# Optimization experiments

Hardware: AMD Instinct MI355X
Metric: run time of the kernel (lower is better)

## Reference

```python
import jax, jax.numpy as jnp
import numpy as np

D_MODEL = 1024
N_HEADS = 16
HEAD_DIM = D_MODEL // N_HEADS
Q_PROJ = D_MODEL // 2
KV_PROJ = D_MODEL
INIT_SCALE = 0.02
EPS = 1e-5


def _ln(x, g, b):
    mu = jnp.mean(x, axis=-1, keepdims=True)
    var = jnp.mean(jnp.square(x - mu), axis=-1, keepdims=True)
    return (x - mu) * jax.lax.rsqrt(var + EPS) * g + b


def setup_inputs() -> dict:
    key = jax.random.key(0)
    ks = jax.random.split(key, 8)
    B, S = 2, 2048
    x = jax.random.normal(ks[0], (B, S, D_MODEL), dtype=jnp.float32)
    W_dq = INIT_SCALE * jax.random.normal(ks[1], (D_MODEL, Q_PROJ), dtype=jnp.float32)
    W_uq = INIT_SCALE * jax.random.normal(ks[2], (Q_PROJ, D_MODEL), dtype=jnp.float32)
    W_dkv = INIT_SCALE * jax.random.normal(ks[3], (D_MODEL, KV_PROJ), dtype=jnp.float32)
    W_ukv = INIT_SCALE * jax.random.normal(ks[4], (KV_PROJ, 2 * D_MODEL), dtype=jnp.float32)
    wo = INIT_SCALE * jax.random.normal(ks[5], (D_MODEL, D_MODEL), dtype=jnp.float32)
    return {
        "x": x,
        "W_dq": W_dq, "W_uq": W_uq,
        "q_ln_g": jnp.ones((Q_PROJ,), jnp.float32), "q_ln_b": jnp.zeros((Q_PROJ,), jnp.float32),
        "W_dkv": W_dkv, "W_ukv": W_ukv,
        "kv_ln_g": jnp.ones((KV_PROJ,), jnp.float32), "kv_ln_b": jnp.zeros((KV_PROJ,), jnp.float32),
        "preq_g": jnp.ones((D_MODEL,), jnp.float32), "preq_b": jnp.zeros((D_MODEL,), jnp.float32),
        "prekv_g": jnp.ones((D_MODEL,), jnp.float32), "prekv_b": jnp.zeros((D_MODEL,), jnp.float32),
        "wo": wo,
    }


def reference(x, W_dq, W_uq, q_ln_g, q_ln_b, W_dkv, W_ukv, kv_ln_g, kv_ln_b,
              preq_g, preq_b, prekv_g, prekv_b, wo):
    B, S, D = x.shape
    H, dh = N_HEADS, HEAD_DIM
    # Q path: pre-norm -> low-rank down -> LN -> up
    x_q = _ln(x, preq_g, preq_b)
    cq = _ln(x_q @ W_dq, q_ln_g, q_ln_b)            # [B,S,D/2]
    Q = (cq @ W_uq).reshape(B, S, H, dh)             # [B,S,H,dh]
    Q = Q / jnp.sqrt(jnp.asarray(dh, x.dtype))
    # KV path: pre-norm -> compress -> LN -> up, split into K,V
    x_kv = _ln(x, prekv_g, prekv_b)
    ckv = _ln(x_kv @ W_dkv, kv_ln_g, kv_ln_b)        # [B,S,D]
    KV = ckv @ W_ukv                                 # [B,S,2D]
    K, V = jnp.split(KV, 2, axis=-1)
    K = K.reshape(B, S, H, dh)
    V = V.reshape(B, S, H, dh)
    # causal attention (scores materialized as in original)
    scores = jnp.einsum('bqhd,bkhd->bhqk', Q, K)     # [B,H,S,S]
    causal = jnp.tril(jnp.ones((S, S), dtype=bool))  # True where allowed
    scores = jnp.where(causal[None, None], scores, jnp.asarray(-jnp.inf, scores.dtype))
    attn = jax.nn.softmax(scores, axis=-1)
    out = jnp.einsum('bhqk,bkhd->bqhd', attn, V).reshape(B, S, D)
    return out @ wo.T
```

## Files before the change

kernel.cpp:

```cpp
#include <hip/hip_runtime.h>
#include <hip/hip_bf16.h>

#define SEQ   2048
#define BATCH 2
#define NROWS 4096
#define DM    1024
#define NHEAD 16
#define DH    64
#define QP    512
#define KVP   1024
#define CH    8

typedef unsigned short us;
typedef ushort4 us4;
using bf16x8 = __attribute__((ext_vector_type(8))) __bf16;
using f32x4  = __attribute__((ext_vector_type(4))) float;

__device__ __forceinline__ us f2bf(float f) {
  union { __hip_bfloat16 h; us u; } cv;
  cv.h = __float2bfloat16(f);
  return cv.u;
}
__device__ __forceinline__ float bf2f(us u) {
  union { unsigned int u32; float f; } cv;
  cv.u32 = ((unsigned int)u) << 16;
  return cv.f;
}
__device__ __forceinline__ float loadp(const void* p, long i, int isbf) {
  return isbf ? bf2f(((const us*)p)[i]) : ((const float*)p)[i];
}
__device__ __forceinline__ void async16(const void* g, void* l) {
  __builtin_amdgcn_global_load_lds((__attribute__((address_space(1))) void*)g,
                                   (__attribute__((address_space(3))) void*)l,
                                   16, 0, 0);
}

__global__ void detect_dtype(const us* __restrict__ xu, int* __restrict__ flag,
                             float4* __restrict__ zsmall, int nz4) {
  __shared__ int red[256];
  const int tid = threadIdx.x;
  const float4 z = {0.f, 0.f, 0.f, 0.f};
  for (int i = tid; i < nz4; i += 256) zsmall[i] = z;
  int cnt = 0;
  for (int i = tid; i < 4096; i += 256) {
    const int e = (xu[i] >> 7) & 0xff;
    if (e == 0 || (e >= 100 && e <= 134)) cnt++;
  }
  red[tid] = cnt;
  __syncthreads();
  for (int s = 128; s; s >>= 1) {
    if (tid < s) red[tid] += red[tid + s];
    __syncthreads();
  }
  if (tid == 0) *flag = (red[0] >= 3900) ? 1 : 0;
}

struct TD { const void* in; us* out; int R, C, nt, trans;
            const void* g; const void* b; float* u; float* c; };

__global__ __launch_bounds__(256) void stage0(
    TD t0, TD t1, TD t2, TD t3, TD t4,
    float4* __restrict__ zp, int n4,
    const void* __restrict__ xin,
    const void* __restrict__ g1, const void* __restrict__ b1,
    const void* __restrict__ g2, const void* __restrict__ b2,
    us* __restrict__ out1, us* __restrict__ out2,
    const int* __restrict__ flag)
{
  __shared__ us tile[32][33];
  __shared__ float red[8];
  __shared__ float musd[2];
  const int tid = threadIdx.x;
  const int isbf = *flag;
  int lin = blockIdx.x;

  if (lin < 5120) {
    TD t = t0;
    if (lin >= t.nt) { lin -= t.nt; t = t1;
      if (lin >= t.nt) { lin -= t.nt; t = t2;
        if (lin >= t.nt) { lin -= t.nt; t = t3;
          if (lin >= t.nt) { lin -= t.nt; t = t4; } } } }
    const int ntx = t.C >> 5;
    const int by = lin / ntx, bx = lin - by * ntx;
    const int tx = tid & 31, ty = tid >> 5;
    const long r0 = (long)by * 32, c0 = (long)bx * 32;
    if (t.trans) {
#pragma unroll
      for (int i = 0; i < 32; i += 8)
        tile[ty + i][tx] = isbf ? ((const us*)t.in)[(r0 + ty + i) * t.C + c0 + tx]
                                : f2bf(((const float*)t.in)[(r0 + ty + i) * t.C + c0 + tx]);
      __syncthreads();
      if (t.g) {
        const float gw = loadp(t.g, r0 + tx, isbf);
#pragma unroll
        for (int i = 0; i < 32; i += 8)
          t.out[(c0 + ty + i) * t.R + r0 + tx] = f2bf(bf2f(tile[tx][ty + i]) * gw);
        if (ty == 0) {
          float up = 0.f, cp = 0.f;
          for (int r = 0; r < 32; r++) {
            const float w = bf2f(tile[r][tx]);
            up += loadp(t.g, r0 + r, isbf) * w;
            cp += loadp(t.b, r0 + r, isbf) * w;
          }
          atomicAdd(&t.u[c0 + tx], up);
          atomicAdd(&t.c[c0 + tx], cp);
        }
      } else {
#pragma unroll
        for (int i = 0; i < 32; i += 8)
          t.out[(c0 + ty + i) * t.R + r0 + tx] = tile[tx][ty + i];
      }
    } else {
#pragma unroll
      for (int i = 0; i < 32; i += 8)
        t.out[(r0 + ty + i) * t.C + c0 + tx] =
            isbf ? ((const us*)t.in)[(r0 + ty + i) * t.C + c0 + tx]
                 : f2bf(((const float*)t.in)[(r0 + ty + i) * t.C + c0 + tx]);
    }
    return;
  }
  if (lin < 6144) {
    const float4 z = {0.f, 0.f, 0.f, 0.f};
    for (int i = (lin - 5120) * 256 + tid; i < n4; i += 1024 * 256) zp[i] = z;
    return;
  }
  const long row = lin - 6144;
  float v[4];
  float s = 0.f, s2 = 0.f;
#pragma unroll
  for (int i = 0; i < 4; i++) {
    const long c = tid + i * 256;
    const float t = loadp(xin, row * 1024 + c, isbf);
    v[i] = t; s += t; s2 += t * t;
  }
#pragma unroll
  for (int off = 32; off > 0; off >>= 1) {
    s  += __shfl_down(s,  off);
    s2 += __shfl_down(s2, off);
  }
  const int wave = tid >> 6, lane = tid & 63;
  if (lane == 0) { red[wave] = s; red[4 + wave] = s2; }
  __syncthreads();
  if (tid == 0) {
    const float ts = red[0] + red[1] + red[2] + red[3];
    const float t2 = red[4] + red[5] + red[6] + red[7];
    const float mu = ts * (1.f / 1024.f);
    const float var = t2 * (1.f / 1024.f) - mu * mu;
    musd[0] = mu; musd[1] = rsqrtf(var + 1e-5f);
  }
  __syncthreads();
  const float mu = musd[0], rs = musd[1];
#pragma unroll
  for (int i = 0; i < 4; i++) {
    const long c = tid + i * 256;
    const float nrm = (v[i] - mu) * rs;
    out1[row * 1024 + c] = f2bf(nrm * loadp(g1, c, isbf) + loadp(b1, c, isbf));
    out2[row * 1024 + c] = f2bf(nrm * loadp(g2, c, isbf) + loadp(b2, c, isbf));
  }
}

struct GD { const us* A; const us* Bt; void* C; int N, K, nxs; float scale; int omode;
            float* S1; float* S2; const float* u; const float* cv; us* C2; };

__global__ __launch_bounds__(256) void gemm_mt(GD g0, GD g1, int nb0,
                                               const int* __restrict__ flag) {
  __shared__ us As[2][128 * 32];
  __shared__ us Bs[2][128 * 32];
  GD g;
  int lin = blockIdx.x;
  if (lin < nb0) g = g0; else { g = g1; lin -= nb0; }
  const int by = lin >> g.nxs;
  const int bx = lin - (by << g.nxs);
  const int N = g.N, K = g.K;

  const int tid  = threadIdx.x;
  const int lane = tid & 63;
  const int wave = tid >> 6;
  const int n16  = lane & 15;
  const int quad = lane >> 4;
  const long m0 = (long)by * 128;
  const long n0 = (long)bx * 128;
  const int wm = (wave >> 1) * 64;
  const int wn = (wave & 1) * 64;

  const f32x4 zero = {0.f, 0.f, 0.f, 0.f};
  f32x4 acc[4][4];
#pragma unroll
  for (int i = 0; i < 4; i++)
#pragma unroll
    for (int j = 0; j < 4; j++) acc[i][j] = zero;

  const int srow = tid >> 2;
  const int scol = (tid & 3) * 8;
  const us* Ag0 = g.A  + (m0 + srow) * K + scol;
  const us* Ag1 = g.A  + (m0 + 64 + srow) * K + scol;
  const us* Bg0 = g.Bt + (n0 + srow) * K + scol;
  const us* Bg1 = g.Bt + (n0 + 64 + srow) * K + scol;
  const int lds_off = srow * 32 + scol;

  for (int k0 = 0; k0 < K; k0 += 64) {
#pragma unroll
    for (int s = 0; s < 2; s++) {
      const int ks = k0 + s * 32;
      async16(Ag0 + ks, As[s] + lds_off);
      async16(Ag1 + ks, As[s] + 2048 + lds_off);
      async16(Bg0 + ks, Bs[s] + lds_off);
      async16(Bg1 + ks, Bs[s] + 2048 + lds_off);
    }
    __syncthreads();
#pragma unroll
    for (int s = 0; s < 2; s++) {
      bf16x8 af[4], bfv[4];
#pragma unroll
      for (int i = 0; i < 4; i++)
        af[i] = *(const bf16x8*)(As[s] + (wm + i * 16 + n16) * 32 + quad * 8);
#pragma unroll
      for (int j = 0; j < 4; j++)
        bfv[j] = *(const bf16x8*)(Bs[s] + (wn + j * 16 + n16) * 32 + quad * 8);
#pragma unroll
      for (int i = 0; i < 4; i++)
#pragma unroll
        for (int j = 0; j < 4; j++)
          acc[i][j] = __builtin_amdgcn_mfma_f32_16x16x32_bf16(af[i], bfv[j], acc[i][j], 0, 0, 0);
    }
    __syncthreads();
  }

  const int om = g.omode;
  us* Cb = (us*)g.C;

  if (om == 4) {
    float s1a[4][4], s2a[4][4];
#pragma unroll
    for (int i = 0; i < 4; i++)
#pragma unroll
      for (int r = 0; r < 4; r++) { s1a[i][r] = 0.f; s2a[i][r] = 0.f; }
#pragma unroll
    for (int i = 0; i < 4; i++) {
      const long row = m0 + wm + i * 16 + quad * 4;
#pragma unroll
      for (int j = 0; j < 4; j++) {
        const long col = n0 + wn + j * 16 + n16;
#pragma unroll
        for (int r = 0; r < 4; r++) {
          const float v = acc[i][j][r] * g.scale;
          Cb[(row + r) * N + col] = f2bf(v);
          s1a[i][r] += v;
          s2a[i][r] += v * v;
        }
      }
    }
#pragma unroll
    for (int i = 0; i < 4; i++)
#pragma unroll
      for (int r = 0; r < 4; r++) {
        float a = s1a[i][r], b = s2a[i][r];
#pragma unroll
        for (int off = 1; off < 16; off <<= 1) {
          a += __shfl_xor(a, off);
          b += __shfl_xor(b, off);
        }
        if (n16 == 0) {
          const long row = m0 + wm + i * 16 + quad * 4 + r;
          atomicAdd(&g.S1[row], a);
          atomicAdd(&g.S2[row], b);
        }
      }
    return;
  }

  if (om == 5 || om == 6) {
    const float invK = 1.f / (float)K;
    float rsr[4][4], mur[4][4];
#pragma unroll
    for (int i = 0; i < 4; i++) {
      const long row = m0 + wm + i * 16 + quad * 4;
#pragma unroll
      for (int r = 0; r < 4; r++) {
        const float s1 = g.S1[row + r];
        const float s2 = g.S2[row + r];
        const float mu = s1 * invK;
        const float var = s2 * invK - mu * mu;
        const float rs = rsqrtf(var + 1e-5f);
        rsr[i][r] = rs;
        mur[i][r] = mu * rs;
      }
    }
    const bool vhalf = (om == 6) && (n0 >= 1024);
#pragma unroll
    for (int i = 0; i < 4; i++) {
      const long rowb = m0 + wm + i * 16 + quad * 4;
#pragma unroll
      for (int j = 0; j < 4; j++) {
        const long col = n0 + wn + j * 16 + n16;
        const float uu = g.u[col];
        const float cc = g.cv[col];
        if (!vhalf) {
          const int nst = (om == 6) ? 1024 : N;
#pragma unroll
          for (int r = 0; r < 4; r++) {
            const float v = g.scale * (rsr[i][r] * acc[i][j][r] - mur[i][r] * uu + cc);
            Cb[(rowb + r) * nst + col] = f2bf(v);
          }
        } else {
          const int bbq = (int)(rowb >> 11);
          const int key = (int)(rowb & 2047);
          const int dimg = (int)col - 1024;
          us4 pk;
          pk.x = f2bf(g.scale * (rsr[i][0] * acc[i][j][0] - mur[i][0] * uu + cc));
          pk.y = f2bf(g.scale * (rsr[i][1] * acc[i][j][1] - mur[i][1] * uu + cc));
          pk.z = f2bf(g.scale * (rsr[i][2] * acc[i][j][2] - mur[i][2] * uu + cc));
          pk.w = f2bf(g.scale * (rsr[i][3] * acc[i][j][3] - mur[i][3] * uu + cc));
          *(us4*)(g.C2 + ((long)(bbq * 1024 + dimg)) * 2048 + key) = pk;
        }
      }
    }
    return;
  }

  const bool obf = (om == 1) || (om == 2 && *flag != 0);
  float* Cf = (float*)g.C;
#pragma unroll
  for (int i = 0; i < 4; i++) {
    const long row = m0 + wm + i * 16 + quad * 4;
#pragma unroll
    for (int j = 0; j < 4; j++) {
      const long col = n0 + wn + j * 16 + n16;
#pragma unroll
      for (int r = 0; r < 4; r++) {
        const float v = acc[i][j][r] * g.scale;
        if (obf) Cb[(row + r) * N + col] = f2bf(v);
        else     Cf[(row + r) * N + col] = v;
      }
    }
  }
}

__global__ __launch_bounds__(256) void flash_attn(
    const us* __restrict__ Kbuf, const us* __restrict__ VT,
    const us* __restrict__ Q,
    float* __restrict__ Oacc, float* __restrict__ Lacc)
{
  __shared__ us Ks[64 * 72];
  __shared__ us Vt[64 * 72];
  __shared__ us Ps[4][32 * 72];

  int lin = blockIdx.x;
  int qt = 15, nc = 0;
  for (; qt >= 0; --qt) { nc = ((2 * qt + 1) >> 3) + 1; if (lin < nc) break; lin -= nc; }
  const int kt0 = lin * CH;
  const int kt1 = min(kt0 + CH, 2 * qt + 2);

  const int h   = blockIdx.y;
  const int bb  = blockIdx.z;
  const int tid = threadIdx.x;
  const int lane = tid & 63;
  const int wave = tid >> 6;
  const int n16 = lane & 15;
  const int quad = lane >> 4;
  const int qbase = qt * 128;
  const long rowQ0 = (long)bb * SEQ;

  bf16x8 aq[2][2];
#pragma unroll
  for (int rg = 0; rg < 2; rg++) {
    const long gq = (rowQ0 + qbase + wave * 32 + rg * 16 + n16) * DM + h * DH;
    aq[rg][0] = *(const bf16x8*)(Q + gq + quad * 8);
    aq[rg][1] = *(const bf16x8*)(Q + gq + 32 + quad * 8);
  }

  const f32x4 zero = {0.f, 0.f, 0.f, 0.f};
  f32x4 oacc[2][4];
#pragma unroll
  for (int rg = 0; rg < 2; rg++)
#pragma unroll
    for (int d = 0; d < 4; d++) oacc[rg][d] = zero;
  float rsum[2] = {0.f, 0.f};

  const int kk_key = tid >> 3;
  const int kk_d8  = (tid & 7) * 8;
  const int vd  = tid & 63;
  const int vkb = (tid >> 6) * 8;

  const us* kgb = Kbuf + (rowQ0 + kk_key) * 1024 + h * DH + kk_d8;
  const us* vtb = VT + ((long)bb * 1024 + h * DH + vd) * 2048;

  uint4 kpre0, kpre1, vpre0, vpre1;
  auto loadKV = [&](int kt) {
    const us* kg = kgb + (long)kt * (64 * 1024);
    kpre0 = *(const uint4*)kg;
    kpre1 = *(const uint4*)(kg + 32 * 1024);
    const us* vg = vtb + kt * 64 + vkb;
    vpre0 = *(const uint4*)vg;
    vpre1 = *(const uint4*)(vg + 32);
  };
  loadKV(kt0);

  us* Pw = Ps[wave];
  const int qw = qbase + wave * 32;

  for (int kt = kt0; kt < kt1; kt++) {
    const int kb = kt * 64;
    __syncthreads();
    *(uint4*)(Ks + kk_key * 72 + kk_d8)        = kpre0;
    *(uint4*)(Ks + (kk_key + 32) * 72 + kk_d8) = kpre1;
    *(uint4*)(Vt + vd * 72 + vkb)              = vpre0;
    *(uint4*)(Vt + vd * 72 + vkb + 32)         = vpre1;
    __syncthreads();
    if (kt + 1 < kt1) loadKV(kt + 1);

    if (kb > qw + 31) continue;

    f32x4 sv[2][4];
#pragma unroll
    for (int j = 0; j < 4; j++) {
      const bf16x8 ak0 = *(const bf16x8*)(Ks + (j * 16 + n16) * 72 + quad * 8);
      const bf16x8 ak1 = *(const bf16x8*)(Ks + (j * 16 + n16) * 72 + 32 + quad * 8);
#pragma unroll
      for (int rg = 0; rg < 2; rg++) {
        f32x4 s = zero;
        s = __builtin_amdgcn_mfma_f32_16x16x32_bf16(ak0, aq[rg][0], s, 0, 0, 0);
        s = __builtin_amdgcn_mfma_f32_16x16x32_bf16(ak1, aq[rg][1], s, 0, 0, 0);
        sv[rg][j] = s;
      }
    }

#pragma unroll
    for (int rg = 0; rg < 2; rg++) {
      if (kb + 63 > qw + rg * 16) {
        const int qg = qw + rg * 16 + n16;
#pragma unroll
        for (int j = 0; j < 4; j++) {
          const int kl = kb + j * 16 + quad * 4;
#pragma unroll
          for (int r = 0; r < 4; r++)
            sv[rg][j][r] = (kl + r <= qg) ? sv[rg][j][r] : -1e30f;
        }
      }
#pragma unroll
      for (int j = 0; j < 4; j++) {
        const float p0 = __builtin_amdgcn_exp2f(sv[rg][j][0]);
        const float p1 = __builtin_amdgcn_exp2f(sv[rg][j][1]);
        const float p2 = __builtin_amdgcn_exp2f(sv[rg][j][2]);
        const float p3 = __builtin_amdgcn_exp2f(sv[rg][j][3]);
        rsum[rg] += (p0 + p1) + (p2 + p3);
        us4 pk;
        pk.x = f2bf(p0); pk.y = f2bf(p1); pk.z = f2bf(p2); pk.w = f2bf(p3);
        *(us4*)(Pw + (rg * 16 + n16) * 72 + j * 16 + quad * 4) = pk;
      }
    }
    __asm__ volatile("s_waitcnt lgkmcnt(0)" ::: "memory");

#pragma unroll
    for (int rg = 0; rg < 2; rg++)
#pragma unroll
      for (int kc = 0; kc < 2; kc++) {
        const bf16x8 ap = *(const bf16x8*)(Pw + (rg * 16 + n16) * 72 + kc * 32 + quad * 8);
#pragma unroll
        for (int d = 0; d < 4; d++) {
          const bf16x8 bv = *(const bf16x8*)(Vt + (d * 16 + n16) * 72 + kc * 32 + quad * 8);
          oacc[rg][d] = __builtin_amdgcn_mfma_f32_16x16x32_bf16(ap, bv, oacc[rg][d], 0, 0, 0);
        }
      }
  }

#pragma unroll
  for (int rg = 0; rg < 2; rg++) {
    float rs = rsum[rg];
    rs += __shfl_xor(rs, 16);
    rs += __shfl_xor(rs, 32);
    const long rw0 = rowQ0 + qbase + wave * 32 + rg * 16;
    if (quad == 0)
      atomicAdd(&Lacc[(rw0 + n16) * NHEAD + h], rs);
#pragma unroll
    for (int r = 0; r < 4; r++) {
      float* dst = Oacc + (rw0 + quad * 4 + r) * DM + h * DH + n16;
#pragma unroll
      for (int d = 0; d < 4; d++)
        atomicAdd(dst + d * 16, oacc[rg][d][r]);
    }
  }
}

__global__ __launch_bounds__(256) void flash_combine(
    const float* __restrict__ Oacc, const float* __restrict__ Lacc,
    us* __restrict__ O)
{
  __shared__ float invl[NHEAD];
  const long row = blockIdx.x;
  const int tid = threadIdx.x;
  if (tid < NHEAD) invl[tid] = 1.f / Lacc[row * NHEAD + tid];
  __syncthreads();
#pragma unroll
  for (int i = 0; i < 4; i++) {
    const int col = tid + i * 256;
    O[row * DM + col] = f2bf(Oacc[row * DM + col] * invl[col >> 6]);
  }
}

extern "C" void kernel_launch(void* const* d_in, const int* in_sizes, int n_in,
                              void* d_out, int out_size, void* d_ws, size_t ws_size,
                              hipStream_t stream) {
  const void* x      = d_in[0];
  const void* Wdq    = d_in[1];
  const void* Wuq    = d_in[2];
  const void* qg     = d_in[3];
  const void* qb     = d_in[4];
  const void* Wdkv   = d_in[5];
  const void* Wukv   = d_in[6];
  const void* kvg    = d_in[7];
  const void* kvb    = d_in[8];
  const void* preqg  = d_in[9];
  const void* preqb  = d_in[10];
  const void* prekvg = d_in[11];
  const void* prekvb = d_in[12];
  const void* wo     = d_in[13];

  char* ws = (char*)d_ws;
  const long MB = 1 << 20;
  int* flag = (int*)ws;
  float* S1q  = (float*)(ws + 4096);
  float* S2q  = S1q + 4096;
  float* S1kv = S2q + 4096;
  float* S2kv = S1kv + 4096;
  float* u2q  = S2kv + 4096;
  float* c2q  = u2q + 1024;
  float* u2kv = c2q + 1024;
  float* c2kv = u2kv + 2048;
  const int nz4 = (4 * 4096 + 2 * 1024 + 2 * 2048) / 4;

  us* wdq_t   = (us*)(ws + 1 * MB);
  us* wuq_t   = (us*)(ws + 2 * MB);
  us* wdkv_t  = (us*)(ws + 3 * MB);
  us* wukv_t  = (us*)(ws + 5 * MB);
  us* wo_c    = (us*)(ws + 9 * MB);
  us* xq      = (us*)(ws + 11 * MB);
  us* xkv     = (us*)(ws + 19 * MB);
  float* Oacc = (float*)(ws + 27 * MB);
  float* Lacc = (float*)(ws + 43 * MB);
  us* obuf    = (us*)(ws + 43 * MB + 256 * 1024);
  us* tq_bf   = obuf;
  us* qbuf    = (us*)(ws + 43 * MB + 256 * 1024 + 8 * MB);
  us* tkv_bf  = (us*)(ws + 43 * MB + 256 * 1024 + 16 * MB);
  us* Kbuf    = (us*)(ws + 43 * MB + 256 * 1024 + 24 * MB);
  us* VT      = (us*)(ws + 43 * MB + 256 * 1024 + 32 * MB);

  detect_dtype<<<1, 256, 0, stream>>>((const us*)x, flag, (float4*)S1q, nz4);

  {
    TD t0 = { Wdq,  wdq_t,  1024,  512,  512, 1, nullptr, nullptr, nullptr, nullptr };
    TD t1 = { Wuq,  wuq_t,   512, 1024,  512, 1, qg,  qb,  u2q,  c2q  };
    TD t2 = { Wdkv, wdkv_t, 1024, 1024, 1024, 1, nullptr, nullptr, nullptr, nullptr };
    TD t3 = { Wukv, wukv_t, 1024, 2048, 2048, 1, kvg, kvb, u2kv, c2kv };
    TD t4 = { wo,   wo_c,   1024, 1024, 1024, 0, nullptr, nullptr, nullptr, nullptr };
    const int n4 = (16 * 1024 * 1024 + 256 * 1024) / 16;
    stage0<<<10240, 256, 0, stream>>>(t0, t1, t2, t3, t4,
                                      (float4*)Oacc, n4,
                                      x, preqg, preqb, prekvg, prekvb, xq, xkv, flag);
  }

  {
    GD g0 = { xq,  wdq_t,  tq_bf,   512, 1024, 2, 1.f, 4, S1q,  S2q,  nullptr, nullptr, nullptr };
    GD g1 = { xkv, wdkv_t, tkv_bf, 1024, 1024, 3, 1.f, 4, S1kv, S2kv, nullptr, nullptr, nullptr };
    gemm_mt<<<384, 256, 0, stream>>>(g0, g1, 128, flag);
  }

  {
    GD g0 = { tq_bf,  wuq_t,  qbuf, 1024,  512, 3, 0.125f * 1.44269504f, 5,
              S1q,  S2q,  u2q,  c2q,  nullptr };
    GD g1 = { tkv_bf, wukv_t, Kbuf, 2048, 1024, 4, 1.f, 6,
              S1kv, S2kv, u2kv, c2kv, VT };
    gemm_mt<<<768, 256, 0, stream>>>(g0, g1, 256, flag);
  }

  flash_attn<<<dim3(40, NHEAD, BATCH), 256, 0, stream>>>(Kbuf, VT, qbuf, Oacc, Lacc);
  flash_combine<<<NROWS, 256, 0, stream>>>(Oacc, Lacc, obuf);

  {
    GD g0 = { obuf, wo_c, d_out, 1024, 1024, 3, 1.f, 2,
              nullptr, nullptr, nullptr, nullptr, nullptr };
    gemm_mt<<<256, 256, 0, stream>>>(g0, g0, 256, flag);
  }
}
```

Baseline: 288.8 us.

## Halve GEMM M-tile, shrink flash-attn split chunk, dedicate blocks for LN-fold sums

The GEMM tile drops from 128x128 to 64x128 and every grid is doubled, so more blocks are available to fill the CUs. Flash attention's key-chunk size falls from 8 to 4, which raises the split-K block count from 40 to 72 per head and batch. The per-column u/c weight sums used for the LayerNorm fold now come from 48 dedicated blocks instead of atomicAdd-based partials in the transpose tiles, so the zeroing of those buffers is dropped. bf16 conversion switches to a hand-written round-half-up bit trick. The trade-offs are less data reuse per GEMM tile, more partial outputs to combine, and slightly different rounding (no round-to-even, no NaN handling).

```diff
diff --git a/kernel.cpp b/kernel.cpp
--- a/kernel.cpp
+++ b/kernel.cpp
@@ -9,7 +9,7 @@
 #define DH    64
 #define QP    512
 #define KVP   1024
-#define CH    8
+#define CH    4
 
 typedef unsigned short us;
 typedef ushort4 us4;
@@ -17,13 +17,12 @@
 using f32x4  = __attribute__((ext_vector_type(4))) float;
 
 __device__ __forceinline__ us f2bf(float f) {
-  union { __hip_bfloat16 h; us u; } cv;
-  cv.h = __float2bfloat16(f);
-  return cv.u;
+  union { float f; unsigned u; } c; c.f = f;
+  return (us)((c.u + 0x8000u) >> 16);
 }
 __device__ __forceinline__ float bf2f(us u) {
-  union { unsigned int u32; float f; } cv;
-  cv.u32 = ((unsigned int)u) << 16;
+  union { unsigned u32; float f; } cv;
+  cv.u32 = ((unsigned)u) << 16;
   return cv.f;
 }
 __device__ __forceinline__ float loadp(const void* p, long i, int isbf) {
@@ -70,10 +69,42 @@
   __shared__ us tile[32][33];
   __shared__ float red[8];
   __shared__ float musd[2];
+  __shared__ float ucred[2][4][64];
   const int tid = threadIdx.x;
   const int isbf = *flag;
   int lin = blockIdx.x;
 
+  if (lin < 48) {
+    TD t = (lin < 16) ? t1 : t3;
+    const int blk = (lin < 16) ? lin : lin - 16;
+    const int Cr = t.R;
+    const int Nc = t.C;
+    const int colx = tid & 63, cseg = tid >> 6;
+    const int col = blk * 64 + colx;
+    const int rows = Cr >> 2;
+    const int r0 = cseg * rows;
+    float usum = 0.f, csum = 0.f;
+    for (int cc = 0; cc < rows; cc += 8) {
+#pragma unroll
+      for (int k = 0; k < 8; k++) {
+        const long rr = r0 + cc + k;
+        const float w = loadp(t.in, rr * Nc + col, isbf);
+        usum += loadp(t.g, rr, isbf) * w;
+        csum += loadp(t.b, rr, isbf) * w;
+      }
+    }
+    ucred[0][cseg][colx] = usum;
+    ucred[1][cseg][colx] = csum;
+    __syncthreads();
+    if (tid < 64)
+      t.u[blk * 64 + tid] = ucred[0][0][tid] + ucred[0][1][tid] + ucred[0][2][tid] + ucred[0][3][tid];
+    else if (tid < 128) {
+      const int tt = tid - 64;
+      t.c[blk * 64 + tt] = ucred[1][0][tt] + ucred[1][1][tt] + ucred[1][2][tt] + ucred[1][3][tt];
+    }
+    return;
+  }
+  lin -= 48;
   if (lin < 5120) {
     TD t = t0;
     if (lin >= t.nt) { lin -= t.nt; t = t1;
@@ -95,16 +126,6 @@
 #pragma unroll
         for (int i = 0; i < 32; i += 8)
           t.out[(c0 + ty + i) * t.R + r0 + tx] = f2bf(bf2f(tile[tx][ty + i]) * gw);
-        if (ty == 0) {
-          float up = 0.f, cp = 0.f;
-          for (int r = 0; r < 32; r++) {
-            const float w = bf2f(tile[r][tx]);
-            up += loadp(t.g, r0 + r, isbf) * w;
-            cp += loadp(t.b, r0 + r, isbf) * w;
-          }
-          atomicAdd(&t.u[c0 + tx], up);
-          atomicAdd(&t.c[c0 + tx], cp);
-        }
       } else {
 #pragma unroll
         for (int i = 0; i < 32; i += 8)
@@ -164,7 +185,7 @@
 
 __global__ __launch_bounds__(256) void gemm_mt(GD g0, GD g1, int nb0,
                                                const int* __restrict__ flag) {
-  __shared__ us As[2][128 * 32];
+  __shared__ us As[2][64 * 32];
   __shared__ us Bs[2][128 * 32];
   GD g;
   int lin = blockIdx.x;
@@ -178,22 +199,21 @@
   const int wave = tid >> 6;
   const int n16  = lane & 15;
   const int quad = lane >> 4;
-  const long m0 = (long)by * 128;
+  const long m0 = (long)by * 64;
   const long n0 = (long)bx * 128;
-  const int wm = (wave >> 1) * 64;
+  const int wm = (wave >> 1) * 32;
   const int wn = (wave & 1) * 64;
 
   const f32x4 zero = {0.f, 0.f, 0.f, 0.f};
-  f32x4 acc[4][4];
-#pragma unroll
-  for (int i = 0; i < 4; i++)
+  f32x4 acc[2][4];
+#pragma unroll
+  for (int i = 0; i < 2; i++)
 #pragma unroll
     for (int j = 0; j < 4; j++) acc[i][j] = zero;
 
   const int srow = tid >> 2;
   const int scol = (tid & 3) * 8;
-  const us* Ag0 = g.A  + (m0 + srow) * K + scol;
-  const us* Ag1 = g.A  + (m0 + 64 + srow) * K + scol;
+  const us* Ag  = g.A  + (m0 + srow) * K + scol;
   const us* Bg0 = g.Bt + (n0 + srow) * K + scol;
   const us* Bg1 = g.Bt + (n0 + 64 + srow) * K + scol;
   const int lds_off = srow * 32 + scol;
@@ -202,23 +222,22 @@
 #pragma unroll
     for (int s = 0; s < 2; s++) {
       const int ks = k0 + s * 32;
-      async16(Ag0 + ks, As[s] + lds_off);
-      async16(Ag1 + ks, As[s] + 2048 + lds_off);
+      async16(Ag  + ks, As[s] + lds_off);
       async16(Bg0 + ks, Bs[s] + lds_off);
       async16(Bg1 + ks, Bs[s] + 2048 + lds_off);
     }
     __syncthreads();
 #pragma unroll
     for (int s = 0; s < 2; s++) {
-      bf16x8 af[4], bfv[4];
-#pragma unroll
-      for (int i = 0; i < 4; i++)
+      bf16x8 af[2], bfv[4];
+#pragma unroll
+      for (int i = 0; i < 2; i++)
         af[i] = *(const bf16x8*)(As[s] + (wm + i * 16 + n16) * 32 + quad * 8);
 #pragma unroll
       for (int j = 0; j < 4; j++)
         bfv[j] = *(const bf16x8*)(Bs[s] + (wn + j * 16 + n16) * 32 + quad * 8);
 #pragma unroll
-      for (int i = 0; i < 4; i++)
+      for (int i = 0; i < 2; i++)
 #pragma unroll
         for (int j = 0; j < 4; j++)
           acc[i][j] = __builtin_amdgcn_mfma_f32_16x16x32_bf16(af[i], bfv[j], acc[i][j], 0, 0, 0);
@@ -230,13 +249,13 @@
   us* Cb = (us*)g.C;
 
   if (om == 4) {
-    float s1a[4][4], s2a[4][4];
-#pragma unroll
-    for (int i = 0; i < 4; i++)
+    float s1a[2][4], s2a[2][4];
+#pragma unroll
+    for (int i = 0; i < 2; i++)
 #pragma unroll
       for (int r = 0; r < 4; r++) { s1a[i][r] = 0.f; s2a[i][r] = 0.f; }
 #pragma unroll
-    for (int i = 0; i < 4; i++) {
+    for (int i = 0; i < 2; i++) {
       const long row = m0 + wm + i * 16 + quad * 4;
 #pragma unroll
       for (int j = 0; j < 4; j++) {
@@ -251,7 +270,7 @@
       }
     }
 #pragma unroll
-    for (int i = 0; i < 4; i++)
+    for (int i = 0; i < 2; i++)
 #pragma unroll
       for (int r = 0; r < 4; r++) {
         float a = s1a[i][r], b = s2a[i][r];
@@ -271,9 +290,9 @@
 
   if (om == 5 || om == 6) {
     const float invK = 1.f / (float)K;
-    float rsr[4][4], mur[4][4];
-#pragma unroll
-    for (int i = 0; i < 4; i++) {
+    float rsr[2][4], mur[2][4];
+#pragma unroll
+    for (int i = 0; i < 2; i++) {
       const long row = m0 + wm + i * 16 + quad * 4;
 #pragma unroll
       for (int r = 0; r < 4; r++) {
@@ -288,7 +307,7 @@
     }
     const bool vhalf = (om == 6) && (n0 >= 1024);
 #pragma unroll
-    for (int i = 0; i < 4; i++) {
+    for (int i = 0; i < 2; i++) {
       const long rowb = m0 + wm + i * 16 + quad * 4;
 #pragma unroll
       for (int j = 0; j < 4; j++) {
@@ -321,7 +340,7 @@
   const bool obf = (om == 1) || (om == 2 && *flag != 0);
   float* Cf = (float*)g.C;
 #pragma unroll
-  for (int i = 0; i < 4; i++) {
+  for (int i = 0; i < 2; i++) {
     const long row = m0 + wm + i * 16 + quad * 4;
 #pragma unroll
     for (int j = 0; j < 4; j++) {
@@ -347,7 +366,7 @@
 
   int lin = blockIdx.x;
   int qt = 15, nc = 0;
-  for (; qt >= 0; --qt) { nc = ((2 * qt + 1) >> 3) + 1; if (lin < nc) break; lin -= nc; }
+  for (; qt >= 0; --qt) { nc = (2 * qt + 5) >> 2; if (lin < nc) break; lin -= nc; }
   const int kt0 = lin * CH;
   const int kt1 = min(kt0 + CH, 2 * qt + 2);
 
@@ -527,7 +546,7 @@
   float* c2q  = u2q + 1024;
   float* u2kv = c2q + 1024;
   float* c2kv = u2kv + 2048;
-  const int nz4 = (4 * 4096 + 2 * 1024 + 2 * 2048) / 4;
+  const int nz4 = (4 * 4096) / 4;
 
   us* wdq_t   = (us*)(ws + 1 * MB);
   us* wuq_t   = (us*)(ws + 2 * MB);
@@ -554,7 +573,7 @@
     TD t3 = { Wukv, wukv_t, 1024, 2048, 2048, 1, kvg, kvb, u2kv, c2kv };
     TD t4 = { wo,   wo_c,   1024, 1024, 1024, 0, nullptr, nullptr, nullptr, nullptr };
     const int n4 = (16 * 1024 * 1024 + 256 * 1024) / 16;
-    stage0<<<10240, 256, 0, stream>>>(t0, t1, t2, t3, t4,
+    stage0<<<10288, 256, 0, stream>>>(t0, t1, t2, t3, t4,
                                       (float4*)Oacc, n4,
                                       x, preqg, preqb, prekvg, prekvb, xq, xkv, flag);
   }
@@ -562,7 +581,7 @@
   {
     GD g0 = { xq,  wdq_t,  tq_bf,   512, 1024, 2, 1.f, 4, S1q,  S2q,  nullptr, nullptr, nullptr };
     GD g1 = { xkv, wdkv_t, tkv_bf, 1024, 1024, 3, 1.f, 4, S1kv, S2kv, nullptr, nullptr, nullptr };
-    gemm_mt<<<384, 256, 0, stream>>>(g0, g1, 128, flag);
+    gemm_mt<<<768, 256, 0, stream>>>(g0, g1, 256, flag);
   }
 
   {
@@ -570,15 +589,15 @@
               S1q,  S2q,  u2q,  c2q,  nullptr };
     GD g1 = { tkv_bf, wukv_t, Kbuf, 2048, 1024, 4, 1.f, 6,
               S1kv, S2kv, u2kv, c2kv, VT };
-    gemm_mt<<<768, 256, 0, stream>>>(g0, g1, 256, flag);
-  }
-
-  flash_attn<<<dim3(40, NHEAD, BATCH), 256, 0, stream>>>(Kbuf, VT, qbuf, Oacc, Lacc);
+    gemm_mt<<<1536, 256, 0, stream>>>(g0, g1, 512, flag);
+  }
+
+  flash_attn<<<dim3(72, NHEAD, BATCH), 256, 0, stream>>>(Kbuf, VT, qbuf, Oacc, Lacc);
   flash_combine<<<NROWS, 256, 0, stream>>>(Oacc, Lacc, obuf);
 
   {
     GD g0 = { obuf, wo_c, d_out, 1024, 1024, 3, 1.f, 2,
               nullptr, nullptr, nullptr, nullptr, nullptr };
-    gemm_mt<<<256, 256, 0, stream>>>(g0, g0, 256, flag);
-  }
-}
+    gemm_mt<<<512, 256, 0, stream>>>(g0, g0, 512, flag);
+  }
+}
```

New measurement: 308.6 us. +6.9%, slower.
